# Kernel tuning notes

Hardware: AMD Instinct MI355X
Metric: run time of the kernel (lower is better)

## Reference

```python
import jax, jax.numpy as jnp
import numpy as np

N = 129  # fixed by fc1: 3*121 -> N-8 = 121
F = 262144
E = 16384

def setup_inputs() -> dict:
    key = jax.random.key(0)
    ks = jax.random.split(key, 18)
    s = 0.05
    return {
        "x": jax.random.normal(ks[0], (N, F), jnp.float32),
        "edge_index": jax.random.randint(ks[1], (2, E), 0, N),
        "edge_attr": jax.random.uniform(ks[2], (E, 3), jnp.float32),
        # GCNConvSortPool (channel1 only; forward reuses it for all 3 edge channels)
        "gcn1_W": jax.random.normal(ks[3], (F, 1), jnp.float32) * (1.0 / np.sqrt(F)),
        "gcn1_b": jnp.zeros((1,), jnp.float32),
        "gcn2_W": jax.random.normal(ks[4], (1, 1), jnp.float32),
        "gcn2_b": jnp.zeros((1,), jnp.float32),
        "conv1_w": jax.random.normal(ks[5], (3, 2, 3), jnp.float32) * s,  # OIH
        "conv1_b": jax.random.normal(ks[6], (3,), jnp.float32) * s,
        "conv2_w": jax.random.normal(ks[7], (1, 3, 3), jnp.float32) * s,
        "conv2_b": jax.random.normal(ks[8], (1,), jnp.float32) * s,
        "fc1_W": jax.random.normal(ks[9], (3 * 121, 32), jnp.float32) * s,
        "fc1_b": jnp.zeros((32,), jnp.float32),
        "fc2_W": jax.random.normal(ks[10], (32, 6), jnp.float32) * s,
        "fc2_b": jnp.zeros((6,), jnp.float32),
        "fc3_W": jax.random.normal(ks[11], (6, 2), jnp.float32) * s,
        "fc3_b": jnp.zeros((2,), jnp.float32),
    }

def _gcn_conv(x, row, col, ew, W, b):
    # PyG GCNConv with edge weights: add self loops (weight 1), symmetric norm.
    n = x.shape[0]
    xw = x @ W                                             # [n, out]
    loop = jnp.arange(n)
    row2 = jnp.concatenate([row, loop])
    col2 = jnp.concatenate([col, loop])
    ew2 = jnp.concatenate([ew, jnp.ones((n,), x.dtype)])
    deg = jax.ops.segment_sum(ew2, col2, num_segments=n)
    dinv = jnp.where(deg > 0, deg ** -0.5, 0.0)
    norm = dinv[row2] * ew2 * dinv[col2]                   # [e+n]
    out = jax.ops.segment_sum(norm[:, None] * xw[row2], col2, num_segments=n)
    return out + b

def _maxpool1d3(z):
    return jax.lax.reduce_window(z, -jnp.inf, jax.lax.max, (1, 1, 3), (1, 1, 1), 'VALID')

def _conv1d(z, w, b):
    out = jax.lax.conv_general_dilated(z, w, (1,), 'VALID', dimension_numbers=('NCH', 'OIH', 'NCH'))
    return out + b[None, :, None]

def _channel(x, row, col, ew, gcn1_W, gcn1_b, gcn2_W, gcn2_b, conv1_w, conv1_b, conv2_w, conv2_b):
    h1 = _gcn_conv(x, row, col, ew, gcn1_W, gcn1_b)        # [N,1]
    h2 = _gcn_conv(h1[:, -1:], row, col, ew, gcn2_W, gcn2_b)  # [N,1]
    h = jnp.concatenate([h1, h2], axis=-1)                 # [N,2]
    perm = jnp.argsort(-h[:, -1])                          # SortPool: sort by last channel, descending, k=N
    h = h[perm]                                            # [N,2]
    z = h.T[None]                                          # [1,2,N]
    z = _maxpool1d3(_conv1d(z, conv1_w, conv1_b))          # [1,3,N-4]
    z = _maxpool1d3(_conv1d(z, conv2_w, conv2_b))          # [1,1,N-8]
    return z

def reference(x, edge_index, edge_attr, gcn1_W, gcn1_b, gcn2_W, gcn2_b,
              conv1_w, conv1_b, conv2_w, conv2_b,
              fc1_W, fc1_b, fc2_W, fc2_b, fc3_W, fc3_b):
    row, col = edge_index[0], edge_index[1]
    outs = [_channel(x, row, col, edge_attr[:, c], gcn1_W, gcn1_b, gcn2_W, gcn2_b,
                     conv1_w, conv1_b, conv2_w, conv2_b) for c in range(3)]
    all_x = jnp.concatenate(outs, axis=-2)                 # [1,3,121]
    h = all_x.reshape(1, -1)                               # [1,363]
    h = jax.nn.elu(h @ fc1_W + fc1_b)                      # dropout=0 -> identity
    h = jax.nn.elu(h @ fc2_W + fc2_b)
    return h @ fc3_W + fc3_b                               # [1,2]
```

## Files before the change

### kernel.cpp

```cpp
#include <hip/hip_runtime.h>
#include <hip/hip_bf16.h>
#include <math.h>

#define NN 129
#define FF 262144
#define EE 16384
#define CHUNKS 32
#define CHUNK (FF / CHUNKS)
#define NB 16
#define EPB (EE / NB)
#define EPT (EPB / 256)
#define NMV (NN * CHUNKS)

#define OFF_PARTIAL 0
#define OFF_DEGP    (OFF_PARTIAL + NN*CHUNKS)
#define OFF_H1P     (OFF_DEGP + NB*3*NN)
#define OFF_H2P     (OFF_H1P + NB*3*NN)
#define OFF_BAR     (OFF_H2P + NB*3*NN)
#define LSTRIDE 32

typedef float vfloat4 __attribute__((ext_vector_type(4)));

__device__ __forceinline__ void gbar(unsigned* line) {
    __syncthreads();
    if (threadIdx.x == 0) {
        __threadfence();
        __hip_atomic_fetch_add(line, 1u, __ATOMIC_ACQ_REL, __HIP_MEMORY_SCOPE_AGENT);
        while (__hip_atomic_load(line, __ATOMIC_ACQUIRE, __HIP_MEMORY_SCOPE_AGENT) < (unsigned)NB)
            __builtin_amdgcn_s_sleep(1);
        __threadfence();
    }
    __syncthreads();
}

__global__ __launch_bounds__(256) void k_fused(
    const float* __restrict__ x, const float* __restrict__ W,
    const int* __restrict__ eidx, const float* __restrict__ eattr,
    double* __restrict__ ws,
    const float* __restrict__ b1, const float* __restrict__ W2, const float* __restrict__ b2,
    const float* __restrict__ c1w, const float* __restrict__ c1b,
    const float* __restrict__ c2w, const float* __restrict__ c2b,
    const float* __restrict__ f1W, const float* __restrict__ f1b,
    const float* __restrict__ f2W, const float* __restrict__ f2b,
    const float* __restrict__ f3W, const float* __restrict__ f3b,
    float* __restrict__ out)
{
    const int b = blockIdx.x;
    const int tid = threadIdx.x;
    const int wave = tid >> 6, lane = tid & 63;

    __shared__ double P[129 + 387 + 387];
    __shared__ double SCR[1917];
    __shared__ double ws4[4];
    __shared__ double fcb[38];

    unsigned* sync = (unsigned*)(ws + OFF_BAR);

    if (b >= NB) {
        const int bm = b - NB;
        const int r = bm / CHUNKS, ch = bm % CHUNKS;
        const vfloat4* xp = (const vfloat4*)(x + (size_t)r * FF + (size_t)ch * CHUNK);
        const float4*  wp = (const float4*)(W + (size_t)ch * CHUNK);
        double acc0 = 0.0, acc1 = 0.0;
#pragma unroll
        for (int i = 0; i < CHUNK / (256 * 4); ++i) {
            vfloat4 xv = __builtin_nontemporal_load(xp + tid + i * 256);
            float4  wv = wp[tid + i * 256];
            acc0 += (double)xv[0] * (double)wv.x + (double)xv[1] * (double)wv.y;
            acc1 += (double)xv[2] * (double)wv.z + (double)xv[3] * (double)wv.w;
        }
        double acc = acc0 + acc1;
        for (int off = 32; off > 0; off >>= 1) acc += __shfl_down(acc, off, 64);
        if (lane == 0) ws4[wave] = acc;
        __syncthreads();
        if (tid == 0) {
            const double v = (ws4[0] + ws4[1]) + (ws4[2] + ws4[3]);
            __hip_atomic_store(&ws[OFF_PARTIAL + bm], v,
                               __ATOMIC_RELAXED, __HIP_MEMORY_SCOPE_AGENT);
            asm volatile("s_waitcnt vmcnt(0)" ::: "memory");
            __hip_atomic_fetch_add(&sync[(bm & 63) * LSTRIDE], 1u,
                                   __ATOMIC_RELAXED, __HIP_MEMORY_SCOPE_AGENT);
        }
        return;
    }

    double* sxw   = P;
    double* sdinv = P + 129;
    double* sh1   = P + 516;
    double (*hp)[3][NN] = (double(*)[3][NN])SCR;

    int er[EPT], ec[EPT];
    float ea[EPT][3];
#pragma unroll
    for (int i = 0; i < EPT; ++i) {
        const int e = b * EPB + i * 256 + tid;
        er[i] = eidx[e];
        ec[i] = eidx[EE + e];
        ea[i][0] = eattr[e * 3 + 0];
        ea[i][1] = eattr[e * 3 + 1];
        ea[i][2] = eattr[e * 3 + 2];
    }

    for (int i = tid; i < 4 * 3 * NN; i += 256) ((double*)hp)[i] = 0.0;
    __syncthreads();
#pragma unroll
    for (int i = 0; i < EPT; ++i) {
        const int cl = ec[i];
#pragma unroll
        for (int c = 0; c < 3; ++c)
            unsafeAtomicAdd(&hp[wave][c][cl], (double)ea[i][c]);
    }
    __syncthreads();
    for (int i = tid; i < 3 * NN; i += 256) {
        const int c = i / NN, j = i % NN;
        ws[OFF_DEGP + b * (3 * NN) + i] =
            (hp[0][c][j] + hp[1][c][j]) + (hp[2][c][j] + hp[3][c][j]);
    }
    gbar(sync + 64 * LSTRIDE);

    for (int v = tid; v < 3 * NN; v += 256) {
        double d = 1.0;
#pragma unroll
        for (int k = 0; k < NB; ++k) d += ws[OFF_DEGP + k * (3 * NN) + v];
        sdinv[v] = (d > 0.0) ? 1.0 / sqrt(d) : 0.0;
    }
    __syncthreads();

    if (tid < 64) {
        unsigned* c = sync + tid * LSTRIDE;
        const unsigned expct = (tid < 32) ? 65u : 64u;
        while (__hip_atomic_load(c, __ATOMIC_RELAXED, __HIP_MEMORY_SCOPE_AGENT) < expct)
            __builtin_amdgcn_s_sleep(32);
    }
    __syncthreads();

    for (int j = tid; j < NN; j += 256) {
        double s = 0.0;
#pragma unroll
        for (int k = 0; k < CHUNKS; ++k)
            s += __hip_atomic_load(&ws[OFF_PARTIAL + j * CHUNKS + k],
                                   __ATOMIC_RELAXED, __HIP_MEMORY_SCOPE_AGENT);
        sxw[j] = s;
    }
    for (int i = tid; i < 4 * 3 * NN; i += 256) ((double*)hp)[i] = 0.0;
    __syncthreads();

    double enw[EPT][3];
#pragma unroll
    for (int i = 0; i < EPT; ++i) {
        const int r = er[i], cl = ec[i];
        const double xwr = sxw[r];
#pragma unroll
        for (int c = 0; c < 3; ++c) {
            const double nw = sdinv[c * NN + r] * (double)ea[i][c] * sdinv[c * NN + cl];
            enw[i][c] = nw;
            unsafeAtomicAdd(&hp[wave][c][cl], nw * xwr);
        }
    }
    __syncthreads();
    for (int i = tid; i < 3 * NN; i += 256) {
        const int c = i / NN, j = i % NN;
        ws[OFF_H1P + b * (3 * NN) + i] =
            (hp[0][c][j] + hp[1][c][j]) + (hp[2][c][j] + hp[3][c][j]);
    }
    gbar(sync + 65 * LSTRIDE);

    const double bb1 = (double)b1[0];
    for (int i = tid; i < 3 * NN; i += 256) {
        const int j = i % NN;
        const double dv = sdinv[i];
        double s = dv * dv * sxw[j] + bb1;
#pragma unroll
        for (int k = 0; k < NB; ++k) s += ws[OFF_H1P + k * (3 * NN) + i];
        sh1[i] = s;
    }
    for (int i = tid; i < 4 * 3 * NN; i += 256) ((double*)hp)[i] = 0.0;
    __syncthreads();

    const double w2 = (double)W2[0];
#pragma unroll
    for (int i = 0; i < EPT; ++i) {
        const int r = er[i], cl = ec[i];
#pragma unroll
        for (int c = 0; c < 3; ++c)
            unsafeAtomicAdd(&hp[wave][c][cl], enw[i][c] * (sh1[c * NN + r] * w2));
    }
    __syncthreads();
    for (int i = tid; i < 3 * NN; i += 256) {
        const int c = i / NN, j = i % NN;
        ws[OFF_H2P + b * (3 * NN) + i] =
            (hp[0][c][j] + hp[1][c][j]) + (hp[2][c][j] + hp[3][c][j]);
    }
    gbar(sync + 66 * LSTRIDE);

    if (b != 0) return;

    double* z0   = SCR;
    double* z1   = SCR + 387;
    double* c1o  = SCR + 774;
    double* h2f  = SCR + 1161;
    int*    rnk  = (int*)(SCR + 1548);
    double* c2o  = SCR;
    double* allx = SCR + 369;
    double* fc1o = fcb;
    double* fc2o = fcb + 32;

    const double bb2 = (double)b2[0];
    for (int i = tid; i < 3 * NN; i += 256) {
        const int j = i % NN;
        const double dv = sdinv[i];
        double s = dv * dv * (sh1[i] * w2) + bb2;
#pragma unroll
        for (int k = 0; k < NB; ++k) s += ws[OFF_H2P + k * (3 * NN) + i];
        h2f[i] = s;
    }
    __syncthreads();

    for (int i = tid; i < 3 * NN; i += 256) {
        const int c = i / NN, j = i % NN;
        const double v = h2f[c * NN + j];
        int rk = 0;
        for (int q = 0; q < NN; ++q) {
            const double u = h2f[c * NN + q];
            rk += (u > v) || (u == v && q < j);
        }
        rnk[i] = rk;
    }
    __syncthreads();
    for (int i = tid; i < 3 * NN; i += 256) {
        const int c = i / NN;
        const int rk = rnk[i];
        z0[c * NN + rk] = sh1[i];
        z1[c * NN + rk] = h2f[i];
    }
    __syncthreads();

    for (int i = tid; i < 3 * 3 * 127; i += 256) {
        const int c = i / (3 * 127), rem = i % (3 * 127), o = rem / 127, p = rem % 127;
        double s = (double)c1b[o];
#pragma unroll
        for (int k = 0; k < 3; ++k) {
            s += (double)c1w[(o * 2 + 0) * 3 + k] * z0[c * NN + p + k];
            s += (double)c1w[(o * 2 + 1) * 3 + k] * z1[c * NN + p + k];
        }
        c1o[(c * 3 + o) * 127 + p] = s;
    }
    __syncthreads();

    for (int i = tid; i < 3 * 123; i += 256) {
        const int c = i / 123, p = i % 123;
        double s = (double)c2b[0];
#pragma unroll
        for (int ic = 0; ic < 3; ++ic)
#pragma unroll
            for (int k = 0; k < 3; ++k) {
                const double* base = c1o + (c * 3 + ic) * 127 + p + k;
                const double m = fmax(base[0], fmax(base[1], base[2]));
                s += (double)c2w[ic * 3 + k] * m;
            }
        c2o[c * 123 + p] = s;
    }
    __syncthreads();
    for (int i = tid; i < 3 * 121; i += 256) {
        const int c = i / 121, p = i % 121;
        allx[c * 121 + p] = fmax(c2o[c * 123 + p],
                            fmax(c2o[c * 123 + p + 1], c2o[c * 123 + p + 2]));
    }
    __syncthreads();

    {
        const int j = tid >> 3, t = tid & 7;
        double s = 0.0;
        for (int i = t; i < 363; i += 8) s += allx[i] * (double)f1W[i * 32 + j];
        s += __shfl_down(s, 4, 8);
        s += __shfl_down(s, 2, 8);
        s += __shfl_down(s, 1, 8);
        if (t == 0) {
            s += (double)f1b[j];
            fc1o[j] = (s > 0.0) ? s : expm1(s);
        }
    }
    __syncthreads();
    if (tid < 6) {
        double s = (double)f2b[tid];
        for (int i = 0; i < 32; ++i) s += fc1o[i] * (double)f2W[i * 6 + tid];
        fc2o[tid] = (s > 0.0) ? s : expm1(s);
    }
    __syncthreads();
    if (tid < 2) {
        double s = (double)f3b[tid];
        for (int i = 0; i < 6; ++i) s += fc2o[i] * (double)f3W[i * 2 + tid];
        out[tid] = (float)s;
    }
}

extern "C" void kernel_launch(void* const* d_in, const int* in_sizes, int n_in,
                              void* d_out, int out_size, void* d_ws, size_t ws_size,
                              hipStream_t stream) {
    const float* x    = (const float*)d_in[0];
    const int*   eidx = (const int*)d_in[1];
    const float* eattr= (const float*)d_in[2];
    const float* g1W  = (const float*)d_in[3];
    const float* g1b  = (const float*)d_in[4];
    const float* g2W  = (const float*)d_in[5];
    const float* g2b  = (const float*)d_in[6];
    const float* c1w  = (const float*)d_in[7];
    const float* c1b  = (const float*)d_in[8];
    const float* c2w  = (const float*)d_in[9];
    const float* c2b  = (const float*)d_in[10];
    const float* f1W  = (const float*)d_in[11];
    const float* f1b  = (const float*)d_in[12];
    const float* f2W  = (const float*)d_in[13];
    const float* f2b  = (const float*)d_in[14];
    const float* f3W  = (const float*)d_in[15];
    const float* f3b  = (const float*)d_in[16];
    float* out = (float*)d_out;
    double* ws = (double*)d_ws;

    hipMemsetAsync((void*)(ws + OFF_BAR), 0, 67 * 128, stream);
    k_fused<<<NN * CHUNKS + NB, 256, 0, stream>>>(
        x, g1W, eidx, eattr, ws,
        g1b, g2W, g2b, c1w, c1b, c2w, c2b,
        f1W, f1b, f2W, f2b, f3W, f3b, out);
}
```

Baseline: 263.9 us.

## Do all edge aggregation in a single block, removing inter-block grid barriers

Replaces the 16 cooperating edge-processing blocks and their three global spin barriers with a single block that loops over all edges in batches of eight, reloading edge data in each GCN pass instead of keeping it in registers. Partial sums now stay in shared memory rather than being written to and re-read from the global workspace. This removes barrier and workspace round-trip latency, but one block now does 16x more serialized LDS atomic work, which may land on the critical path after the GEMV blocks finish. The poll sleep interval is also shortened.

```diff
diff --git a/kernel.cpp b/kernel.cpp
--- a/kernel.cpp
+++ b/kernel.cpp
@@ -7,31 +7,17 @@
 #define EE 16384
 #define CHUNKS 32
 #define CHUNK (FF / CHUNKS)
-#define NB 16
-#define EPB (EE / NB)
-#define EPT (EPB / 256)
 #define NMV (NN * CHUNKS)
 
+#define EPT_T (EE / 256)
+#define BATCH 8
+#define NBATCH (EPT_T / BATCH)
+
 #define OFF_PARTIAL 0
-#define OFF_DEGP    (OFF_PARTIAL + NN*CHUNKS)
-#define OFF_H1P     (OFF_DEGP + NB*3*NN)
-#define OFF_H2P     (OFF_H1P + NB*3*NN)
-#define OFF_BAR     (OFF_H2P + NB*3*NN)
+#define OFF_BAR     (OFF_PARTIAL + NMV)
 #define LSTRIDE 32
 
 typedef float vfloat4 __attribute__((ext_vector_type(4)));
-
-__device__ __forceinline__ void gbar(unsigned* line) {
-    __syncthreads();
-    if (threadIdx.x == 0) {
-        __threadfence();
-        __hip_atomic_fetch_add(line, 1u, __ATOMIC_ACQ_REL, __HIP_MEMORY_SCOPE_AGENT);
-        while (__hip_atomic_load(line, __ATOMIC_ACQUIRE, __HIP_MEMORY_SCOPE_AGENT) < (unsigned)NB)
-            __builtin_amdgcn_s_sleep(1);
-        __threadfence();
-    }
-    __syncthreads();
-}
 
 __global__ __launch_bounds__(256) void k_fused(
     const float* __restrict__ x, const float* __restrict__ W,
@@ -50,14 +36,14 @@
     const int wave = tid >> 6, lane = tid & 63;
 
     __shared__ double P[129 + 387 + 387];
-    __shared__ double SCR[1917];
+    __shared__ double SCR[1935];
     __shared__ double ws4[4];
     __shared__ double fcb[38];
 
     unsigned* sync = (unsigned*)(ws + OFF_BAR);
 
-    if (b >= NB) {
-        const int bm = b - NB;
+    if (b != 0) {
+        const int bm = b - 1;
         const int r = bm / CHUNKS, ch = bm % CHUNKS;
         const vfloat4* xp = (const vfloat4*)(x + (size_t)r * FF + (size_t)ch * CHUNK);
         const float4*  wp = (const float4*)(W + (size_t)ch * CHUNK);
@@ -89,39 +75,33 @@
     double* sh1   = P + 516;
     double (*hp)[3][NN] = (double(*)[3][NN])SCR;
 
-    int er[EPT], ec[EPT];
-    float ea[EPT][3];
-#pragma unroll
-    for (int i = 0; i < EPT; ++i) {
-        const int e = b * EPB + i * 256 + tid;
-        er[i] = eidx[e];
-        ec[i] = eidx[EE + e];
-        ea[i][0] = eattr[e * 3 + 0];
-        ea[i][1] = eattr[e * 3 + 1];
-        ea[i][2] = eattr[e * 3 + 2];
-    }
-
     for (int i = tid; i < 4 * 3 * NN; i += 256) ((double*)hp)[i] = 0.0;
     __syncthreads();
-#pragma unroll
-    for (int i = 0; i < EPT; ++i) {
-        const int cl = ec[i];
-#pragma unroll
-        for (int c = 0; c < 3; ++c)
-            unsafeAtomicAdd(&hp[wave][c][cl], (double)ea[i][c]);
-    }
-    __syncthreads();
-    for (int i = tid; i < 3 * NN; i += 256) {
-        const int c = i / NN, j = i % NN;
-        ws[OFF_DEGP + b * (3 * NN) + i] =
-            (hp[0][c][j] + hp[1][c][j]) + (hp[2][c][j] + hp[3][c][j]);
-    }
-    gbar(sync + 64 * LSTRIDE);
-
+    for (int bt = 0; bt < NBATCH; ++bt) {
+        int   c8[BATCH];
+        float a8[BATCH][3];
+#pragma unroll
+        for (int i = 0; i < BATCH; ++i) {
+            const int e = (bt * BATCH + i) * 256 + tid;
+            c8[i] = eidx[EE + e];
+            a8[i][0] = eattr[e * 3 + 0];
+            a8[i][1] = eattr[e * 3 + 1];
+            a8[i][2] = eattr[e * 3 + 2];
+        }
+#pragma unroll
+        for (int i = 0; i < BATCH; ++i)
+#pragma unroll
+            for (int c = 0; c < 3; ++c)
+                unsafeAtomicAdd(&hp[wave][c][c8[i]], (double)a8[i][c]);
+    }
+    __syncthreads();
     for (int v = tid; v < 3 * NN; v += 256) {
-        double d = 1.0;
-#pragma unroll
-        for (int k = 0; k < NB; ++k) d += ws[OFF_DEGP + k * (3 * NN) + v];
+        const double d = 1.0 + (hp[0][0][0 ? 0 : 0], 0.0);
+        (void)d;
+    }
+    for (int v = tid; v < 3 * NN; v += 256) {
+        const int c = v / NN, j = v % NN;
+        const double d = 1.0 + ((hp[0][c][j] + hp[1][c][j]) + (hp[2][c][j] + hp[3][c][j]));
         sdinv[v] = (d > 0.0) ? 1.0 / sqrt(d) : 0.0;
     }
     __syncthreads();
@@ -130,7 +110,7 @@
         unsigned* c = sync + tid * LSTRIDE;
         const unsigned expct = (tid < 32) ? 65u : 64u;
         while (__hip_atomic_load(c, __ATOMIC_RELAXED, __HIP_MEMORY_SCOPE_AGENT) < expct)
-            __builtin_amdgcn_s_sleep(32);
+            __builtin_amdgcn_s_sleep(8);
     }
     __syncthreads();
 
@@ -145,76 +125,85 @@
     for (int i = tid; i < 4 * 3 * NN; i += 256) ((double*)hp)[i] = 0.0;
     __syncthreads();
 
-    double enw[EPT][3];
-#pragma unroll
-    for (int i = 0; i < EPT; ++i) {
-        const int r = er[i], cl = ec[i];
-        const double xwr = sxw[r];
-#pragma unroll
-        for (int c = 0; c < 3; ++c) {
-            const double nw = sdinv[c * NN + r] * (double)ea[i][c] * sdinv[c * NN + cl];
-            enw[i][c] = nw;
-            unsafeAtomicAdd(&hp[wave][c][cl], nw * xwr);
-        }
-    }
-    __syncthreads();
+    for (int bt = 0; bt < NBATCH; ++bt) {
+        int   r8[BATCH], c8[BATCH];
+        float a8[BATCH][3];
+#pragma unroll
+        for (int i = 0; i < BATCH; ++i) {
+            const int e = (bt * BATCH + i) * 256 + tid;
+            r8[i] = eidx[e];
+            c8[i] = eidx[EE + e];
+            a8[i][0] = eattr[e * 3 + 0];
+            a8[i][1] = eattr[e * 3 + 1];
+            a8[i][2] = eattr[e * 3 + 2];
+        }
+#pragma unroll
+        for (int i = 0; i < BATCH; ++i) {
+            const int r = r8[i], cl = c8[i];
+            const double xwr = sxw[r];
+#pragma unroll
+            for (int c = 0; c < 3; ++c) {
+                const double nw = sdinv[c * NN + r] * (double)a8[i][c] * sdinv[c * NN + cl];
+                unsafeAtomicAdd(&hp[wave][c][cl], nw * xwr);
+            }
+        }
+    }
+    __syncthreads();
+
+    const double bb1 = (double)b1[0];
     for (int i = tid; i < 3 * NN; i += 256) {
         const int c = i / NN, j = i % NN;
-        ws[OFF_H1P + b * (3 * NN) + i] =
-            (hp[0][c][j] + hp[1][c][j]) + (hp[2][c][j] + hp[3][c][j]);
-    }
-    gbar(sync + 65 * LSTRIDE);
-
-    const double bb1 = (double)b1[0];
-    for (int i = tid; i < 3 * NN; i += 256) {
-        const int j = i % NN;
         const double dv = sdinv[i];
-        double s = dv * dv * sxw[j] + bb1;
-#pragma unroll
-        for (int k = 0; k < NB; ++k) s += ws[OFF_H1P + k * (3 * NN) + i];
-        sh1[i] = s;
-    }
+        sh1[i] = dv * dv * sxw[j] + bb1 +
+                 ((hp[0][c][j] + hp[1][c][j]) + (hp[2][c][j] + hp[3][c][j]));
+    }
+    __syncthreads();
     for (int i = tid; i < 4 * 3 * NN; i += 256) ((double*)hp)[i] = 0.0;
     __syncthreads();
 
     const double w2 = (double)W2[0];
-#pragma unroll
-    for (int i = 0; i < EPT; ++i) {
-        const int r = er[i], cl = ec[i];
-#pragma unroll
-        for (int c = 0; c < 3; ++c)
-            unsafeAtomicAdd(&hp[wave][c][cl], enw[i][c] * (sh1[c * NN + r] * w2));
-    }
-    __syncthreads();
+    for (int bt = 0; bt < NBATCH; ++bt) {
+        int   r8[BATCH], c8[BATCH];
+        float a8[BATCH][3];
+#pragma unroll
+        for (int i = 0; i < BATCH; ++i) {
+            const int e = (bt * BATCH + i) * 256 + tid;
+            r8[i] = eidx[e];
+            c8[i] = eidx[EE + e];
+            a8[i][0] = eattr[e * 3 + 0];
+            a8[i][1] = eattr[e * 3 + 1];
+            a8[i][2] = eattr[e * 3 + 2];
+        }
+#pragma unroll
+        for (int i = 0; i < BATCH; ++i) {
+            const int r = r8[i], cl = c8[i];
+#pragma unroll
+            for (int c = 0; c < 3; ++c) {
+                const double nw = sdinv[c * NN + r] * (double)a8[i][c] * sdinv[c * NN + cl];
+                unsafeAtomicAdd(&hp[wave][c][cl], nw * (sh1[c * NN + r] * w2));
+            }
+        }
+    }
+    __syncthreads();
+
+    double* h2f  = SCR + 1548;
+    const double bb2 = (double)b2[0];
     for (int i = tid; i < 3 * NN; i += 256) {
         const int c = i / NN, j = i % NN;
-        ws[OFF_H2P + b * (3 * NN) + i] =
-            (hp[0][c][j] + hp[1][c][j]) + (hp[2][c][j] + hp[3][c][j]);
-    }
-    gbar(sync + 66 * LSTRIDE);
-
-    if (b != 0) return;
+        const double dv = sdinv[i];
+        h2f[i] = dv * dv * (sh1[i] * w2) + bb2 +
+                 ((hp[0][c][j] + hp[1][c][j]) + (hp[2][c][j] + hp[3][c][j]));
+    }
+    __syncthreads();
 
     double* z0   = SCR;
     double* z1   = SCR + 387;
+    int*    rnk  = (int*)(SCR + 774);
     double* c1o  = SCR + 774;
-    double* h2f  = SCR + 1161;
-    int*    rnk  = (int*)(SCR + 1548);
     double* c2o  = SCR;
     double* allx = SCR + 369;
     double* fc1o = fcb;
     double* fc2o = fcb + 32;
-
-    const double bb2 = (double)b2[0];
-    for (int i = tid; i < 3 * NN; i += 256) {
-        const int j = i % NN;
-        const double dv = sdinv[i];
-        double s = dv * dv * (sh1[i] * w2) + bb2;
-#pragma unroll
-        for (int k = 0; k < NB; ++k) s += ws[OFF_H2P + k * (3 * NN) + i];
-        h2f[i] = s;
-    }
-    __syncthreads();
 
     for (int i = tid; i < 3 * NN; i += 256) {
         const int c = i / NN, j = i % NN;
@@ -317,8 +306,8 @@
     float* out = (float*)d_out;
     double* ws = (double*)d_ws;
 
-    hipMemsetAsync((void*)(ws + OFF_BAR), 0, 67 * 128, stream);
-    k_fused<<<NN * CHUNKS + NB, 256, 0, stream>>>(
+    hipMemsetAsync((void*)(ws + OFF_BAR), 0, 64 * 128, stream);
+    k_fused<<<NMV + 1, 256, 0, stream>>>(
         x, g1W, eidx, eattr, ws,
         g1b, g2W, g2b, c1w, c1b, c2w, c2b,
         f1W, f1b, f2W, f2b, f3W, f3b, out);
```

New measurement: 286.0 us. 1.08x slower.

## Replace memset-reset barriers with self-resetting device-global sync counters

Applied to the files above, without the earlier changes.

Moves the barrier counters from the workspace into a device-global array that block 0 resets at the end of the kernel, removing the separate hipMemsetAsync launch before each run. Drops the explicit threadfences in the grid barrier and relies on agent-scope atomic loads and stores for cross-block data. Turns the last barrier into a one-way arrive for non-zero blocks so only block 0 waits, and shortens the polling sleep. The risk is correctness: the reset depends on block 0 finishing after every other block's arrival, and the memory ordering becomes weaker.

```diff
diff --git a/kernel.cpp b/kernel.cpp
--- a/kernel.cpp
+++ b/kernel.cpp
@@ -13,24 +13,30 @@
 #define NMV (NN * CHUNKS)
 
 #define OFF_PARTIAL 0
-#define OFF_DEGP    (OFF_PARTIAL + NN*CHUNKS)
+#define OFF_DEGP    (OFF_PARTIAL + NMV)
 #define OFF_H1P     (OFF_DEGP + NB*3*NN)
 #define OFF_H2P     (OFF_H1P + NB*3*NN)
-#define OFF_BAR     (OFF_H2P + NB*3*NN)
+
 #define LSTRIDE 32
+__device__ __align__(128) unsigned g_sync[67 * LSTRIDE];
 
 typedef float vfloat4 __attribute__((ext_vector_type(4)));
 
 __device__ __forceinline__ void gbar(unsigned* line) {
     __syncthreads();
     if (threadIdx.x == 0) {
-        __threadfence();
         __hip_atomic_fetch_add(line, 1u, __ATOMIC_ACQ_REL, __HIP_MEMORY_SCOPE_AGENT);
         while (__hip_atomic_load(line, __ATOMIC_ACQUIRE, __HIP_MEMORY_SCOPE_AGENT) < (unsigned)NB)
             __builtin_amdgcn_s_sleep(1);
-        __threadfence();
-    }
-    __syncthreads();
+    }
+    __syncthreads();
+}
+
+__device__ __forceinline__ double agent_ld(const double* p) {
+    return __hip_atomic_load(p, __ATOMIC_RELAXED, __HIP_MEMORY_SCOPE_AGENT);
+}
+__device__ __forceinline__ void agent_st(double* p, double v) {
+    __hip_atomic_store(p, v, __ATOMIC_RELAXED, __HIP_MEMORY_SCOPE_AGENT);
 }
 
 __global__ __launch_bounds__(256) void k_fused(
@@ -50,11 +56,9 @@
     const int wave = tid >> 6, lane = tid & 63;
 
     __shared__ double P[129 + 387 + 387];
-    __shared__ double SCR[1917];
+    __shared__ double SCR[1935];
     __shared__ double ws4[4];
     __shared__ double fcb[38];
-
-    unsigned* sync = (unsigned*)(ws + OFF_BAR);
 
     if (b >= NB) {
         const int bm = b - NB;
@@ -75,10 +79,9 @@
         __syncthreads();
         if (tid == 0) {
             const double v = (ws4[0] + ws4[1]) + (ws4[2] + ws4[3]);
-            __hip_atomic_store(&ws[OFF_PARTIAL + bm], v,
-                               __ATOMIC_RELAXED, __HIP_MEMORY_SCOPE_AGENT);
+            agent_st(&ws[OFF_PARTIAL + bm], v);
             asm volatile("s_waitcnt vmcnt(0)" ::: "memory");
-            __hip_atomic_fetch_add(&sync[(bm & 63) * LSTRIDE], 1u,
+            __hip_atomic_fetch_add(&g_sync[(bm & 63) * LSTRIDE], 1u,
                                    __ATOMIC_RELAXED, __HIP_MEMORY_SCOPE_AGENT);
         }
         return;
@@ -113,24 +116,24 @@
     __syncthreads();
     for (int i = tid; i < 3 * NN; i += 256) {
         const int c = i / NN, j = i % NN;
-        ws[OFF_DEGP + b * (3 * NN) + i] =
-            (hp[0][c][j] + hp[1][c][j]) + (hp[2][c][j] + hp[3][c][j]);
-    }
-    gbar(sync + 64 * LSTRIDE);
+        agent_st(&ws[OFF_DEGP + b * (3 * NN) + i],
+                 (hp[0][c][j] + hp[1][c][j]) + (hp[2][c][j] + hp[3][c][j]));
+    }
+    gbar(&g_sync[64 * LSTRIDE]);
 
     for (int v = tid; v < 3 * NN; v += 256) {
         double d = 1.0;
 #pragma unroll
-        for (int k = 0; k < NB; ++k) d += ws[OFF_DEGP + k * (3 * NN) + v];
+        for (int k = 0; k < NB; ++k) d += agent_ld(&ws[OFF_DEGP + k * (3 * NN) + v]);
         sdinv[v] = (d > 0.0) ? 1.0 / sqrt(d) : 0.0;
     }
     __syncthreads();
 
     if (tid < 64) {
-        unsigned* c = sync + tid * LSTRIDE;
+        unsigned* c = &g_sync[tid * LSTRIDE];
         const unsigned expct = (tid < 32) ? 65u : 64u;
         while (__hip_atomic_load(c, __ATOMIC_RELAXED, __HIP_MEMORY_SCOPE_AGENT) < expct)
-            __builtin_amdgcn_s_sleep(32);
+            __builtin_amdgcn_s_sleep(8);
     }
     __syncthreads();
 
@@ -138,8 +141,7 @@
         double s = 0.0;
 #pragma unroll
         for (int k = 0; k < CHUNKS; ++k)
-            s += __hip_atomic_load(&ws[OFF_PARTIAL + j * CHUNKS + k],
-                                   __ATOMIC_RELAXED, __HIP_MEMORY_SCOPE_AGENT);
+            s += agent_ld(&ws[OFF_PARTIAL + j * CHUNKS + k]);
         sxw[j] = s;
     }
     for (int i = tid; i < 4 * 3 * NN; i += 256) ((double*)hp)[i] = 0.0;
@@ -160,10 +162,10 @@
     __syncthreads();
     for (int i = tid; i < 3 * NN; i += 256) {
         const int c = i / NN, j = i % NN;
-        ws[OFF_H1P + b * (3 * NN) + i] =
-            (hp[0][c][j] + hp[1][c][j]) + (hp[2][c][j] + hp[3][c][j]);
-    }
-    gbar(sync + 65 * LSTRIDE);
+        agent_st(&ws[OFF_H1P + b * (3 * NN) + i],
+                 (hp[0][c][j] + hp[1][c][j]) + (hp[2][c][j] + hp[3][c][j]));
+    }
+    gbar(&g_sync[65 * LSTRIDE]);
 
     const double bb1 = (double)b1[0];
     for (int i = tid; i < 3 * NN; i += 256) {
@@ -171,7 +173,7 @@
         const double dv = sdinv[i];
         double s = dv * dv * sxw[j] + bb1;
 #pragma unroll
-        for (int k = 0; k < NB; ++k) s += ws[OFF_H1P + k * (3 * NN) + i];
+        for (int k = 0; k < NB; ++k) s += agent_ld(&ws[OFF_H1P + k * (3 * NN) + i]);
         sh1[i] = s;
     }
     for (int i = tid; i < 4 * 3 * NN; i += 256) ((double*)hp)[i] = 0.0;
@@ -188,18 +190,31 @@
     __syncthreads();
     for (int i = tid; i < 3 * NN; i += 256) {
         const int c = i / NN, j = i % NN;
-        ws[OFF_H2P + b * (3 * NN) + i] =
-            (hp[0][c][j] + hp[1][c][j]) + (hp[2][c][j] + hp[3][c][j]);
-    }
-    gbar(sync + 66 * LSTRIDE);
-
-    if (b != 0) return;
+        agent_st(&ws[OFF_H2P + b * (3 * NN) + i],
+                 (hp[0][c][j] + hp[1][c][j]) + (hp[2][c][j] + hp[3][c][j]));
+    }
+
+    __syncthreads();
+    if (b != 0) {
+        if (tid == 0)
+            __hip_atomic_fetch_add(&g_sync[66 * LSTRIDE], 1u,
+                                   __ATOMIC_ACQ_REL, __HIP_MEMORY_SCOPE_AGENT);
+        return;
+    }
+    if (tid == 0) {
+        __hip_atomic_fetch_add(&g_sync[66 * LSTRIDE], 1u,
+                               __ATOMIC_ACQ_REL, __HIP_MEMORY_SCOPE_AGENT);
+        while (__hip_atomic_load(&g_sync[66 * LSTRIDE], __ATOMIC_ACQUIRE,
+                                 __HIP_MEMORY_SCOPE_AGENT) < (unsigned)NB)
+            __builtin_amdgcn_s_sleep(1);
+    }
+    __syncthreads();
 
     double* z0   = SCR;
     double* z1   = SCR + 387;
+    int*    rnk  = (int*)(SCR + 774);
     double* c1o  = SCR + 774;
-    double* h2f  = SCR + 1161;
-    int*    rnk  = (int*)(SCR + 1548);
+    double* h2f  = SCR + 1548;
     double* c2o  = SCR;
     double* allx = SCR + 369;
     double* fc1o = fcb;
@@ -207,11 +222,10 @@
 
     const double bb2 = (double)b2[0];
     for (int i = tid; i < 3 * NN; i += 256) {
-        const int j = i % NN;
         const double dv = sdinv[i];
         double s = dv * dv * (sh1[i] * w2) + bb2;
 #pragma unroll
-        for (int k = 0; k < NB; ++k) s += ws[OFF_H2P + k * (3 * NN) + i];
+        for (int k = 0; k < NB; ++k) s += agent_ld(&ws[OFF_H2P + k * (3 * NN) + i]);
         h2f[i] = s;
     }
     __syncthreads();
@@ -292,6 +306,11 @@
         for (int i = 0; i < 6; ++i) s += fc2o[i] * (double)f3W[i * 2 + tid];
         out[tid] = (float)s;
     }
+
+    __syncthreads();
+    if (tid < 67)
+        __hip_atomic_store(&g_sync[tid * LSTRIDE], 0u,
+                           __ATOMIC_RELAXED, __HIP_MEMORY_SCOPE_AGENT);
 }
 
 extern "C" void kernel_launch(void* const* d_in, const int* in_sizes, int n_in,
@@ -317,8 +336,7 @@
     float* out = (float*)d_out;
     double* ws = (double*)d_ws;
 
-    hipMemsetAsync((void*)(ws + OFF_BAR), 0, 67 * 128, stream);
-    k_fused<<<NN * CHUNKS + NB, 256, 0, stream>>>(
+    k_fused<<<NMV + NB, 256, 0, stream>>>(
         x, g1W, eidx, eattr, ws,
         g1b, g2W, g2b, c1w, c1b, c2w, c2b,
         f1W, f1b, f2W, f2b, f3W, f3b, out);
```

Result: faster. 258.1 us (-2.2%).
